# Kernel tuning notes

Measured on AMD Instinct MI355X. Metric: run time of the kernel, lower is better.

The kernel has to match this reference:

```python
import jax, jax.numpy as jnp
import numpy as np
import hashlib

HIDDEN = 256
IN_SIZE = 32
ROUNDS = 64
BATCH = 8192


def _sha256_noise(nonces_u8: np.ndarray) -> np.ndarray:
    # Faithful to generate_noise: sha256 of the 32 nonce bytes gives 256 bits;
    # only indices i < 256 (byte_idx < 32) are set, so only round 0 has noise.
    B = nonces_u8.shape[0]
    noise = np.zeros((B, ROUNDS, HIDDEN), dtype=np.float32)
    for b in range(B):
        h = hashlib.sha256(nonces_u8[b].tobytes()).digest()
        bits = np.unpackbits(np.frombuffer(h, dtype=np.uint8), bitorder='little')
        noise[b, 0, :] = bits.astype(np.float32)
    return noise


def setup_inputs() -> dict:
    key = jax.random.key(0)
    k_nonce, k_mat = jax.random.split(key)
    nonces = jax.random.randint(k_nonce, (BATCH, IN_SIZE), 0, 256, dtype=jnp.int32)
    # Ternary round matrices in {-1, 0, 1}; original derives them from a
    # ChaCha20 keystream mod 3 minus 1 -- same distribution, different PRNG.
    matrices = (jax.random.randint(k_mat, (ROUNDS, HIDDEN, HIDDEN), 0, 3, dtype=jnp.int32) - 1).astype(jnp.float32)
    nonces_u8 = np.asarray(nonces).astype(np.uint8)
    noise = jnp.asarray(_sha256_noise(nonces_u8))  # [B, ROUNDS, HIDDEN]
    return {"nonces": nonces, "matrices": matrices, "noise": noise}


def reference(nonces, matrices, noise):
    B = nonces.shape[0]
    # Vectorized bit-unpack: x[b, i*8 + j] = (nonces[b, i] >> j) & 1
    bits = ((nonces[:, :, None] >> jnp.arange(8, dtype=jnp.int32)) & 1)
    x = bits.reshape(B, IN_SIZE * 8).astype(jnp.float32)  # [B, 256]

    noise_r = jnp.swapaxes(noise, 0, 1)  # [ROUNDS, B, HIDDEN]

    def step(x, mn):
        M, n = mn
        # torch: fmod(matmul(M, x.T).T + noise_r, 2.0) == fmod(x @ M.T + n, 2)
        return jnp.fmod(x @ M.T + n, 2.0), None

    x, _ = jax.lax.scan(step, x, (matrices, noise_r))
    return x
```

## Files before the change

### kernel.cpp

```cpp
#include <hip/hip_runtime.h>


#define ROUNDS 64
#define ROWS   32

typedef __attribute__((ext_vector_type(4))) int    int4v;
typedef __attribute__((ext_vector_type(8))) int    int8v;
typedef __attribute__((ext_vector_type(4))) float  float4v;

struct alignas(16) C16 { char b[16]; };

__device__ __forceinline__ unsigned fp4_code(int v) {
    return ((unsigned)(v & 1) << 1) | (((unsigned)v >> 31) << 3);
}

__global__ void prep_A(const float* __restrict__ M, char* __restrict__ A) {
    int cid  = blockIdx.x * blockDim.x + threadIdx.x;
    int lane = cid & 63;
    int kt   = (cid >> 6) & 1;
    int ht   = (cid >> 7) & 15;
    int r    = cid >> 11;
    int h  = 16 * ht + (lane & 15);
    int k0 = 128 * kt + (lane >> 4) * 32;
    const float* src = M + ((size_t)(r * 256 + h) * 256 + k0);
    C16 w;
#pragma unroll
    for (int j2 = 0; j2 < 16; j2++) {
        int v0 = (int)src[2 * j2];
        int v1 = (int)src[2 * j2 + 1];
        w.b[j2] = (char)(fp4_code(v0) | (fp4_code(v1) << 4));
    }
    *(C16*)(A + (size_t)cid * 16) = w;
}

__device__ __forceinline__ void round_body(
    int r, bool last, bool pre,
    const char* __restrict__ xc, char* __restrict__ xn,
    int4v (&a)[2][2], int4v (&an)[2][2],
    const int4v* __restrict__ Abase,
    const float* __restrict__ noise, float* __restrict__ out,
    int b0, int lane, int wave)
{
    const int l15  = lane & 15;
    const int quad = lane >> 4;

    int4v b[2][2];
#pragma unroll
    for (int bt = 0; bt < 2; bt++) {
        int row = 16 * bt + l15;
#pragma unroll
        for (int kt = 0; kt < 2; kt++) {
            int c = 4 * kt + quad;
            b[bt][kt] = *(const int4v*)&xc[row * 128 + ((c ^ (row & 7)) * 16)];
        }
    }

    if (pre) {
#pragma unroll
        for (int i = 0; i < 2; i++) {
            int ht = 2 * wave + i;
#pragma unroll
            for (int kt = 0; kt < 2; kt++)
                an[i][kt] = Abase[(size_t)((((r + 1) * 16 + ht) * 2 + kt) * 64) + lane];
        }
    }

    float4v acc[2][2];
#pragma unroll
    for (int i = 0; i < 2; i++)
#pragma unroll
        for (int bt = 0; bt < 2; bt++) {
            float4v c = {0.f, 0.f, 0.f, 0.f};
#pragma unroll
            for (int kt = 0; kt < 2; kt++) {
                int8v a8 = {a[i][kt][0], a[i][kt][1], a[i][kt][2], a[i][kt][3], 0, 0, 0, 0};
                int8v b8 = {b[bt][kt][0], b[bt][kt][1], b[bt][kt][2], b[bt][kt][3], 0, 0, 0, 0};
                c = __builtin_amdgcn_mfma_scale_f32_16x16x128_f8f6f4(
                        a8, b8, c, 4, 4, 0, 0x7F7F7F7F, 0, 0x7F7F7F7F);
            }
            acc[i][bt] = c;
        }

#pragma unroll
    for (int i = 0; i < 2; i++) {
        int ht = 2 * wave + i;
#pragma unroll
        for (int bt = 0; bt < 2; bt++) {
            int bb = 16 * bt + l15;
            int v[4];
#pragma unroll
            for (int e = 0; e < 4; e++) v[e] = (int)acc[i][bt][e];
            if (r == 0) {
                float4v nz = *(const float4v*)&noise[(size_t)(b0 + bb) * (ROUNDS * 256)
                                                     + 16 * ht + 4 * quad];
#pragma unroll
                for (int e = 0; e < 4; e++) v[e] += (int)nz[e];
            }
            if (!last) {
                unsigned pk = 0;
#pragma unroll
                for (int e = 0; e < 4; e++)
                    pk |= fp4_code(v[e] % 2) << (4 * e);
                *(unsigned short*)&xn[bb * 128 + (((ht >> 1) ^ (bb & 7)) * 16)
                                      + 8 * (ht & 1) + 2 * quad] = (unsigned short)pk;
            } else {
                float4v o;
#pragma unroll
                for (int e = 0; e < 4; e++) o[e] = (float)(v[e] % 2);
                *(float4v*)&out[(size_t)(b0 + bb) * 256 + 16 * ht + 4 * quad] = o;
            }
        }
    }
    __syncthreads();
}

__global__ __launch_bounds__(512, 2) void tenshash_main(
    const int*   __restrict__ nonces,
    const char*  __restrict__ Afrag,
    const float* __restrict__ noise,
    float*       __restrict__ out)
{
    __shared__ alignas(16) char xbuf[2][ROWS * 128];

    const int tid  = threadIdx.x;
    const int lane = tid & 63;
    const int wave = tid >> 6;
    const int b0 = blockIdx.x * ROWS;

    if (tid < 256) {
        int m = tid >> 3;
        int c = tid & 7;
        const int* np = &nonces[(b0 + m) * 32 + 4 * c];
        C16 w;
#pragma unroll
        for (int p = 0; p < 16; p++) {
            int nw = np[p >> 2];
            int bit0 = (nw >> ((2 * p) & 7)) & 1;
            int bit1 = (nw >> ((2 * p + 1) & 7)) & 1;
            w.b[p] = (char)((bit0 << 1) | (bit1 << 5));
        }
        *(C16*)&xbuf[0][m * 128 + ((c ^ (m & 7)) * 16)] = w;
    }

    const int4v* Abase = (const int4v*)Afrag;
    int4v aA[2][2], aB[2][2];
#pragma unroll
    for (int i = 0; i < 2; i++) {
        int ht = 2 * wave + i;
#pragma unroll
        for (int kt = 0; kt < 2; kt++)
            aA[i][kt] = Abase[(size_t)((ht * 2 + kt) * 64) + lane];
    }
    __syncthreads();

    for (int rr = 0; rr < ROUNDS / 2; rr++) {
        int r0 = 2 * rr;
        round_body(r0,     false,                true,
                   xbuf[0], xbuf[1], aA, aB, Abase, noise, out, b0, lane, wave);
        round_body(r0 + 1, r0 + 1 == ROUNDS - 1, rr < ROUNDS / 2 - 1,
                   xbuf[1], xbuf[0], aB, aA, Abase, noise, out, b0, lane, wave);
    }
}

extern "C" void kernel_launch(void* const* d_in, const int* in_sizes, int n_in,
                              void* d_out, int out_size, void* d_ws, size_t ws_size,
                              hipStream_t stream) {
    const int*   nonces   = (const int*)d_in[0];
    const float* matrices = (const float*)d_in[1];
    const float* noise    = (const float*)d_in[2];
    float* out  = (float*)d_out;
    char* Afrag = (char*)d_ws;

    prep_A<<<512, 256, 0, stream>>>(matrices, Afrag);
    tenshash_main<<<256, 512, 0, stream>>>(nonces, Afrag, noise, out);
}
```

Before: 631.5 us.

## Split hidden tiles across 16 waves per block instead of 8

Each block now launches 1024 threads (16 waves), and each wave computes a single 16-row hidden tile instead of two. This halves the MFMA and epilogue work per wave and gives the latency-bound round chain more wave-level parallelism. In exchange every round's __syncthreads now covers twice as many waves, which adds barrier cost. Launch bounds change to 1024 threads with a minimum of 4 blocks per CU.

```diff
diff --git a/kernel.cpp b/kernel.cpp
--- a/kernel.cpp
+++ b/kernel.cpp
@@ -36,7 +36,7 @@
 __device__ __forceinline__ void round_body(
     int r, bool last, bool pre,
     const char* __restrict__ xc, char* __restrict__ xn,
-    int4v (&a)[2][2], int4v (&an)[2][2],
+    int4v (&a)[2], int4v (&an)[2],
     const int4v* __restrict__ Abase,
     const float* __restrict__ noise, float* __restrict__ out,
     int b0, int lane, int wave)
@@ -57,64 +57,54 @@
 
     if (pre) {
 #pragma unroll
-        for (int i = 0; i < 2; i++) {
-            int ht = 2 * wave + i;
-#pragma unroll
-            for (int kt = 0; kt < 2; kt++)
-                an[i][kt] = Abase[(size_t)((((r + 1) * 16 + ht) * 2 + kt) * 64) + lane];
-        }
+        for (int kt = 0; kt < 2; kt++)
+            an[kt] = Abase[(size_t)((((r + 1) * 16 + wave) * 2 + kt) * 64) + lane];
     }
 
-    float4v acc[2][2];
+    float4v acc[2];
 #pragma unroll
-    for (int i = 0; i < 2; i++)
+    for (int bt = 0; bt < 2; bt++) {
+        float4v c = {0.f, 0.f, 0.f, 0.f};
 #pragma unroll
-        for (int bt = 0; bt < 2; bt++) {
-            float4v c = {0.f, 0.f, 0.f, 0.f};
-#pragma unroll
-            for (int kt = 0; kt < 2; kt++) {
-                int8v a8 = {a[i][kt][0], a[i][kt][1], a[i][kt][2], a[i][kt][3], 0, 0, 0, 0};
-                int8v b8 = {b[bt][kt][0], b[bt][kt][1], b[bt][kt][2], b[bt][kt][3], 0, 0, 0, 0};
-                c = __builtin_amdgcn_mfma_scale_f32_16x16x128_f8f6f4(
-                        a8, b8, c, 4, 4, 0, 0x7F7F7F7F, 0, 0x7F7F7F7F);
-            }
-            acc[i][bt] = c;
+        for (int kt = 0; kt < 2; kt++) {
+            int8v a8 = {a[kt][0], a[kt][1], a[kt][2], a[kt][3], 0, 0, 0, 0};
+            int8v b8 = {b[bt][kt][0], b[bt][kt][1], b[bt][kt][2], b[bt][kt][3], 0, 0, 0, 0};
+            c = __builtin_amdgcn_mfma_scale_f32_16x16x128_f8f6f4(
+                    a8, b8, c, 4, 4, 0, 0x7F7F7F7F, 0, 0x7F7F7F7F);
         }
+        acc[bt] = c;
+    }
 
 #pragma unroll
-    for (int i = 0; i < 2; i++) {
-        int ht = 2 * wave + i;
+    for (int bt = 0; bt < 2; bt++) {
+        int bb = 16 * bt + l15;
+        int v[4];
 #pragma unroll
-        for (int bt = 0; bt < 2; bt++) {
-            int bb = 16 * bt + l15;
-            int v[4];
+        for (int e = 0; e < 4; e++) v[e] = (int)acc[bt][e];
+        if (r == 0) {
+            float4v nz = *(const float4v*)&noise[(size_t)(b0 + bb) * (ROUNDS * 256)
+                                                 + 16 * wave + 4 * quad];
 #pragma unroll
-            for (int e = 0; e < 4; e++) v[e] = (int)acc[i][bt][e];
-            if (r == 0) {
-                float4v nz = *(const float4v*)&noise[(size_t)(b0 + bb) * (ROUNDS * 256)
-                                                     + 16 * ht + 4 * quad];
+            for (int e = 0; e < 4; e++) v[e] += (int)nz[e];
+        }
+        if (!last) {
+            unsigned pk = 0;
 #pragma unroll
-                for (int e = 0; e < 4; e++) v[e] += (int)nz[e];
-            }
-            if (!last) {
-                unsigned pk = 0;
+            for (int e = 0; e < 4; e++)
+                pk |= fp4_code(v[e] % 2) << (4 * e);
+            *(unsigned short*)&xn[bb * 128 + (((wave >> 1) ^ (bb & 7)) * 16)
+                                  + 8 * (wave & 1) + 2 * quad] = (unsigned short)pk;
+        } else {
+            float4v o;
 #pragma unroll
-                for (int e = 0; e < 4; e++)
-                    pk |= fp4_code(v[e] % 2) << (4 * e);
-                *(unsigned short*)&xn[bb * 128 + (((ht >> 1) ^ (bb & 7)) * 16)
-                                      + 8 * (ht & 1) + 2 * quad] = (unsigned short)pk;
-            } else {
-                float4v o;
-#pragma unroll
-                for (int e = 0; e < 4; e++) o[e] = (float)(v[e] % 2);
-                *(float4v*)&out[(size_t)(b0 + bb) * 256 + 16 * ht + 4 * quad] = o;
-            }
+            for (int e = 0; e < 4; e++) o[e] = (float)(v[e] % 2);
+            *(float4v*)&out[(size_t)(b0 + bb) * 256 + 16 * wave + 4 * quad] = o;
         }
     }
     __syncthreads();
 }
 
-__global__ __launch_bounds__(512, 2) void tenshash_main(
+__global__ __launch_bounds__(1024, 4) void tenshash_main(
     const int*   __restrict__ nonces,
     const char*  __restrict__ Afrag,
     const float* __restrict__ noise,
@@ -125,6 +115,7 @@
     const int tid  = threadIdx.x;
     const int lane = tid & 63;
     const int wave = tid >> 6;
+
     const int b0 = blockIdx.x * ROWS;
 
     if (tid < 256) {
@@ -143,14 +134,10 @@
     }
 
     const int4v* Abase = (const int4v*)Afrag;
-    int4v aA[2][2], aB[2][2];
+    int4v aA[2], aB[2];
 #pragma unroll
-    for (int i = 0; i < 2; i++) {
-        int ht = 2 * wave + i;
-#pragma unroll
-        for (int kt = 0; kt < 2; kt++)
-            aA[i][kt] = Abase[(size_t)((ht * 2 + kt) * 64) + lane];
-    }
+    for (int kt = 0; kt < 2; kt++)
+        aA[kt] = Abase[(size_t)((wave * 2 + kt) * 64) + lane];
     __syncthreads();
 
     for (int rr = 0; rr < ROUNDS / 2; rr++) {
@@ -172,5 +159,5 @@
     char* Afrag = (char*)d_ws;
 
     prep_A<<<512, 256, 0, stream>>>(matrices, Afrag);
-    tenshash_main<<<256, 512, 0, stream>>>(nonces, Afrag, noise, out);
+    tenshash_main<<<256, 1024, 0, stream>>>(nonces, Afrag, noise, out);
 }
```

Result: no change. 629.6 us (-0.3%).
